# Kernel tuning notes

Measured on AMD Instinct MI355X. Metric: run time of the kernel, lower is better.

## Reference

```python
import jax, jax.numpy as jnp
import numpy as np

DIM = 3072
HEADS = 24
HEAD_DIM = 128
MLP_HIDDEN = 12288
SEQ = 2048
BATCH = 1
EPS = 1e-6


def setup_inputs() -> dict:
    key = jax.random.key(0)
    ks = jax.random.split(key, 12)
    s = 0.02
    return {
        "hidden_states": jax.random.normal(ks[0], (BATCH, SEQ, DIM), jnp.float32),
        "temb": jax.random.normal(ks[1], (BATCH, DIM), jnp.float32),
        "rope_cos": jax.random.uniform(ks[2], (SEQ, HEAD_DIM), jnp.float32),
        "rope_sin": jax.random.uniform(ks[3], (SEQ, HEAD_DIM), jnp.float32),
        # AdaLN-Zero single: Linear(dim -> 3*dim)
        "norm_w": jax.random.normal(ks[4], (3 * DIM, DIM), jnp.float32) * s,
        "norm_b": jnp.zeros((3 * DIM,), jnp.float32),
        # fused QKV + MLP projection: Linear(dim -> 3*dim + mlp_hidden)
        "qkv_mlp_w": jax.random.normal(ks[5], (3 * DIM + MLP_HIDDEN, DIM), jnp.float32) * s,
        "qkv_mlp_b": jnp.zeros((3 * DIM + MLP_HIDDEN,), jnp.float32),
        # proj_out: Linear(dim + mlp_hidden -> dim)
        "proj_w": jax.random.normal(ks[6], (DIM, DIM + MLP_HIDDEN), jnp.float32) * s,
        "proj_b": jnp.zeros((DIM,), jnp.float32),
        # qk RMSNorm weights (per head_dim)
        "rms_q_w": jnp.ones((HEAD_DIM,), jnp.float32),
        "rms_k_w": jnp.ones((HEAD_DIM,), jnp.float32),
    }


def _rms_norm(x, w):
    # x: [B,S,H,D], normalize over D
    var = jnp.mean(jnp.square(x), axis=-1, keepdims=True)
    return x * jax.lax.rsqrt(var + EPS) * w


def _apply_rope(x, cos, sin):
    # x: [B,S,H,D]; cos/sin: [S,D]. diffusers use_real, unbind_dim=-1 convention.
    xr = x.reshape(*x.shape[:-1], HEAD_DIM // 2, 2)
    rot = jnp.stack([-xr[..., 1], xr[..., 0]], axis=-1).reshape(x.shape)
    c = cos[None, :, None, :]
    s = sin[None, :, None, :]
    return x * c + rot * s


def reference(hidden_states, temb, rope_cos, rope_sin, norm_w, norm_b,
              qkv_mlp_w, qkv_mlp_b, proj_w, proj_b, rms_q_w, rms_k_w):
    B, S, _ = hidden_states.shape
    residual = hidden_states

    # --- AdaLayerNormZeroSingle ---
    mod = jax.nn.silu(temb) @ norm_w.T + norm_b          # [B, 3*dim]
    shift, scale, gate = jnp.split(mod, 3, axis=-1)       # each [B, dim]
    mu = jnp.mean(hidden_states, axis=-1, keepdims=True)
    var = jnp.mean(jnp.square(hidden_states - mu), axis=-1, keepdims=True)
    ln = (hidden_states - mu) * jax.lax.rsqrt(var + EPS)
    norm_h = ln * (1.0 + scale[:, None, :]) + shift[:, None, :]

    # --- fused QKV + MLP GEMM ---
    qkv_mlp = norm_h @ qkv_mlp_w.T + qkv_mlp_b             # [B,S,3*dim+mlp]
    qkv, mlp_h = jnp.split(qkv_mlp, [3 * DIM], axis=-1)
    mlp_out = jax.nn.gelu(mlp_h, approximate=True)         # tanh GELU

    q, k, v = jnp.split(qkv, 3, axis=-1)
    q = q.reshape(B, S, HEADS, HEAD_DIM)
    k = k.reshape(B, S, HEADS, HEAD_DIM)
    v = v.reshape(B, S, HEADS, HEAD_DIM)

    # qk RMSNorm + RoPE
    q = _apply_rope(_rms_norm(q, rms_q_w), rope_cos, rope_sin)
    k = _apply_rope(_rms_norm(k, rms_k_w), rope_cos, rope_sin)

    # scaled dot-product attention
    scale_f = 1.0 / np.sqrt(HEAD_DIM)
    scores = jnp.einsum("bqhd,bkhd->bhqk", q, k) * scale_f
    probs = jax.nn.softmax(scores, axis=-1)
    attn = jnp.einsum("bhqk,bkhd->bqhd", probs, v).reshape(B, S, DIM)

    # proj_out on concat(attn, gelu(mlp)) + gated residual
    cat = jnp.concatenate([attn, mlp_out], axis=-1)        # [B,S,dim+mlp]
    proj = cat @ proj_w.T + proj_b                          # [B,S,dim]
    return gate[:, None, :] * proj + residual
```

## Files before the change

### kernel.cpp

```cpp
#include <hip/hip_runtime.h>
#include <stdint.h>

typedef __bf16 bf16;
typedef __bf16 bf16x8 __attribute__((ext_vector_type(8)));
typedef __bf16 bf16x4 __attribute__((ext_vector_type(4)));
typedef float f32x4 __attribute__((ext_vector_type(4)));

#define DIM   3072
#define SEQ   2048
#define QKVW  9216
#define MLPH  12288
#define FUSED 21504
#define CATW  15360
#define HD    128
#define NH    24

__device__ __forceinline__ void gload_lds16(const void* g, void* l) {
  __builtin_amdgcn_global_load_lds((__attribute__((address_space(1))) void*)g,
                                   (__attribute__((address_space(3))) void*)l,
                                   16, 0, 0);
}

__global__ __launch_bounds__(256) void k_mod_gemv(
    const float* __restrict__ temb, const float* __restrict__ nw,
    const float* __restrict__ nb, float* __restrict__ mod)
{
  int j = blockIdx.x * 4 + (threadIdx.x >> 6);
  int lane = threadIdx.x & 63;
  const float* row = nw + (size_t)j * DIM;
  float acc = 0.f;
  #pragma unroll
  for (int k0 = 0; k0 < DIM; k0 += 256) {
    int k = k0 + lane * 4;
    float4 w = *(const float4*)(row + k);
    float4 t = *(const float4*)(temb + k);
    float s0 = t.x / (1.f + __expf(-t.x));
    float s1 = t.y / (1.f + __expf(-t.y));
    float s2 = t.z / (1.f + __expf(-t.z));
    float s3 = t.w / (1.f + __expf(-t.w));
    acc += w.x * s0 + w.y * s1 + w.z * s2 + w.w * s3;
  }
  #pragma unroll
  for (int m = 32; m >= 1; m >>= 1) acc += __shfl_xor(acc, m, 64);
  if (lane == 0) mod[j] = acc + nb[j];
}

__global__ __launch_bounds__(256) void k_ln_mod(
    const float* __restrict__ hs, const float* __restrict__ mod,
    bf16* __restrict__ nh)
{
  int m = blockIdx.x;
  int t = threadIdx.x;
  const float* x = hs + (size_t)m * DIM;
  float4 v[3];
  float s = 0.f, ss = 0.f;
  #pragma unroll
  for (int i = 0; i < 3; i++) {
    v[i] = *(const float4*)(x + i * 1024 + t * 4);
    s  += v[i].x + v[i].y + v[i].z + v[i].w;
    ss += v[i].x * v[i].x + v[i].y * v[i].y + v[i].z * v[i].z + v[i].w * v[i].w;
  }
  #pragma unroll
  for (int msk = 32; msk >= 1; msk >>= 1) {
    s  += __shfl_xor(s, msk, 64);
    ss += __shfl_xor(ss, msk, 64);
  }
  __shared__ float red[8];
  int wave = t >> 6;
  if ((t & 63) == 0) { red[wave] = s; red[4 + wave] = ss; }
  __syncthreads();
  s  = red[0] + red[1] + red[2] + red[3];
  ss = red[4] + red[5] + red[6] + red[7];
  float mu  = s * (1.f / DIM);
  float var = ss * (1.f / DIM) - mu * mu;
  float rstd = rsqrtf(var + 1e-6f);
  #pragma unroll
  for (int i = 0; i < 3; i++) {
    int col = i * 1024 + t * 4;
    const float* sc = mod + DIM + col;
    const float* sh = mod + col;
    float4 vv = v[i];
    bf16x4 o;
    o[0] = (bf16)((vv.x - mu) * rstd * (1.f + sc[0]) + sh[0]);
    o[1] = (bf16)((vv.y - mu) * rstd * (1.f + sc[1]) + sh[1]);
    o[2] = (bf16)((vv.z - mu) * rstd * (1.f + sc[2]) + sh[2]);
    o[3] = (bf16)((vv.w - mu) * rstd * (1.f + sc[3]) + sh[3]);
    *(bf16x4*)(nh + (size_t)m * DIM + col) = o;
  }
}

__global__ __launch_bounds__(256) void k_cvt(
    const float* __restrict__ s, bf16* __restrict__ d, size_t n)
{
  size_t stride = (size_t)gridDim.x * 256 * 8;
  for (size_t i = ((size_t)blockIdx.x * 256 + threadIdx.x) * 8; i < n; i += stride) {
    float4 a = *(const float4*)(s + i);
    float4 b = *(const float4*)(s + i + 4);
    bf16x8 h;
    h[0] = (bf16)a.x; h[1] = (bf16)a.y; h[2] = (bf16)a.z; h[3] = (bf16)a.w;
    h[4] = (bf16)b.x; h[5] = (bf16)b.y; h[6] = (bf16)b.z; h[7] = (bf16)b.w;
    *(bf16x8*)(d + i) = h;
  }
}

template<int MODE>
__global__ __launch_bounds__(512, 2) void k_gemm8(
    const bf16* __restrict__ A, const bf16* __restrict__ B,
    const float* __restrict__ bias, int K, int ntn, int nkp,
    bf16* __restrict__ oq, bf16* __restrict__ ocat, float* __restrict__ pk)
{
  __shared__ bf16 lds[65536];
  int tid = threadIdx.x;
  int wave = tid >> 6, lane = tid & 63;
  int wm = wave >> 2, wn = wave & 3;

  int nwg = gridDim.x;
  int bid = blockIdx.x;
  int swz = (bid & 7) * (nwg >> 3) + (bid >> 3);
  int mt = swz & 7;
  int rest = swz >> 3;
  int nt = rest % ntn;
  int kc = rest / ntn;
  int m0 = mt * 256, n0 = nt * 256;
  int Kp = K / nkp;
  int kbeg = kc * Kp;
  int NT = Kp >> 6;

  int rb0 = (wave >> 1) * 16 + (lane & 15);
  int cb0 = (wave & 1) * 32 + (lane >> 4) * 8;

  const bf16* Ag = A + (size_t)m0 * K + kbeg;
  const bf16* Bg = B + (size_t)n0 * K + kbeg;

  auto stage = [&](const bf16* g0, int kt, int h, int opb) {
    int kw = kt - (kt >= NT ? NT : 0);
    const bf16* g = g0 + (size_t)(h * 128 + rb0) * K + kw * 64 + cb0;
    bf16* l = &lds[((kt & 1) << 15) + opb + ((h << 4) + wave) * 512];
    gload_lds16(g, l);
    gload_lds16(g + (size_t)64 * K, l + 4096);
  };

  f32x4 acc[8][4];
  #pragma unroll
  for (int i = 0; i < 8; i++)
    #pragma unroll
    for (int j = 0; j < 4; j++) acc[i][j] = (f32x4){0.f, 0.f, 0.f, 0.f};

  stage(Ag, 0, 0, 0);     stage(Ag, 0, 1, 0);
  stage(Bg, 0, 0, 16384); stage(Bg, 0, 1, 16384);
  stage(Ag, 1, 0, 0);     stage(Ag, 1, 1, 0);
  asm volatile("s_waitcnt vmcnt(4)" ::: "memory");
  __builtin_amdgcn_s_barrier();

  const int abase = wm * 16 * 512;
  const int bbase = 16384 + wn * 8 * 512;
  const int lo = lane * 8;
  bf16x8 af[8][2], bfr[4][2];

  for (int kt = 0; kt < NT; kt++) {
    int bo = (kt & 1) << 15;
    #pragma unroll
    for (int mi = 0; mi < 4; mi++)
      #pragma unroll
      for (int ks = 0; ks < 2; ks++)
        af[mi][ks] = *(const bf16x8*)&lds[bo + abase + (mi * 2 + ks) * 512 + lo];
    #pragma unroll
    for (int ni = 0; ni < 2; ni++)
      #pragma unroll
      for (int ks = 0; ks < 2; ks++)
        bfr[ni][ks] = *(const bf16x8*)&lds[bo + bbase + (ni * 2 + ks) * 512 + lo];
    stage(Bg, kt + 1, 0, 16384);
    __builtin_amdgcn_s_barrier();
    asm volatile("s_waitcnt lgkmcnt(0)" ::: "memory");
    __builtin_amdgcn_sched_barrier(0);
    __builtin_amdgcn_s_setprio(1);
    #pragma unroll
    for (int mi = 0; mi < 4; mi++)
      #pragma unroll
      for (int ni = 0; ni < 2; ni++)
        #pragma unroll
        for (int ks = 0; ks < 2; ks++)
          acc[mi][ni] = __builtin_amdgcn_mfma_f32_16x16x32_bf16(af[mi][ks], bfr[ni][ks], acc[mi][ni], 0, 0, 0);
    __builtin_amdgcn_s_setprio(0);
    __builtin_amdgcn_s_barrier();
    #pragma unroll
    for (int mi = 4; mi < 8; mi++)
      #pragma unroll
      for (int ks = 0; ks < 2; ks++)
        af[mi][ks] = *(const bf16x8*)&lds[bo + abase + (mi * 2 + ks) * 512 + lo];
    #pragma unroll
    for (int ni = 2; ni < 4; ni++)
      #pragma unroll
      for (int ks = 0; ks < 2; ks++)
        bfr[ni][ks] = *(const bf16x8*)&lds[bo + bbase + (ni * 2 + ks) * 512 + lo];
    stage(Bg, kt + 1, 1, 16384);
    __builtin_amdgcn_s_barrier();
    asm volatile("s_waitcnt lgkmcnt(0)" ::: "memory");
    __builtin_amdgcn_sched_barrier(0);
    __builtin_amdgcn_s_setprio(1);
    #pragma unroll
    for (int mi = 4; mi < 8; mi++)
      #pragma unroll
      for (int ni = 2; ni < 4; ni++)
        #pragma unroll
        for (int ks = 0; ks < 2; ks++)
          acc[mi][ni] = __builtin_amdgcn_mfma_f32_16x16x32_bf16(af[mi][ks], bfr[ni][ks], acc[mi][ni], 0, 0, 0);
    __builtin_amdgcn_s_setprio(0);
    __builtin_amdgcn_s_barrier();
    stage(Ag, kt + 2, 0, 0);
    __builtin_amdgcn_s_barrier();
    __builtin_amdgcn_sched_barrier(0);
    __builtin_amdgcn_s_setprio(1);
    #pragma unroll
    for (int mi = 0; mi < 4; mi++)
      #pragma unroll
      for (int ni = 2; ni < 4; ni++)
        #pragma unroll
        for (int ks = 0; ks < 2; ks++)
          acc[mi][ni] = __builtin_amdgcn_mfma_f32_16x16x32_bf16(af[mi][ks], bfr[ni][ks], acc[mi][ni], 0, 0, 0);
    __builtin_amdgcn_s_setprio(0);
    __builtin_amdgcn_s_barrier();
    stage(Ag, kt + 2, 1, 0);
    asm volatile("s_waitcnt vmcnt(4)" ::: "memory");
    __builtin_amdgcn_s_barrier();
    __builtin_amdgcn_sched_barrier(0);
    __builtin_amdgcn_s_setprio(1);
    #pragma unroll
    for (int mi = 4; mi < 8; mi++)
      #pragma unroll
      for (int ni = 0; ni < 2; ni++)
        #pragma unroll
        for (int ks = 0; ks < 2; ks++)
          acc[mi][ni] = __builtin_amdgcn_mfma_f32_16x16x32_bf16(af[mi][ks], bfr[ni][ks], acc[mi][ni], 0, 0, 0);
    __builtin_amdgcn_s_setprio(0);
    __builtin_amdgcn_s_barrier();
  }

  int rr = (lane >> 4) * 4, cl = lane & 15;
  int mw0 = m0 + wm * 128, nw0 = n0 + wn * 64;
  #pragma unroll
  for (int mi = 0; mi < 8; mi++) {
    #pragma unroll
    for (int ni = 0; ni < 4; ni++) {
      int n = nw0 + ni * 16 + cl;
      #pragma unroll
      for (int r = 0; r < 4; r++) {
        int m = mw0 + mi * 16 + rr + r;
        float v = acc[mi][ni][r];
        if (MODE == 0) {
          v += bias[n];
          if (n < QKVW) {
            oq[(size_t)m * QKVW + n] = (bf16)v;
          } else {
            float g = 0.5f * v * (1.f + tanhf(0.7978845608028654f * (v + 0.044715f * v * v * v)));
            ocat[(size_t)m * CATW + DIM + (n - QKVW)] = (bf16)g;
          }
        } else {
          pk[(size_t)kc * SEQ * DIM + (size_t)m * DIM + n] = v;
        }
      }
    }
  }
}

template<int MODE>
__global__ __launch_bounds__(256) void k_gemm2(
    const bf16* __restrict__ A, const float* __restrict__ Bf,
    const float* __restrict__ bias, int K, int ntn,
    bf16* __restrict__ oq, bf16* __restrict__ ocat,
    const float* __restrict__ gate, const float* __restrict__ resid,
    float* __restrict__ of)
{
  __shared__ bf16 sA[8192];
  __shared__ bf16 sB[8192];
  int nwg = gridDim.x;
  int bid = blockIdx.x;
  int swz = (bid & 7) * (nwg >> 3) + (bid >> 3);
  int mt = swz & 15, nt = swz >> 4;
  int m0 = mt * 128, n0 = nt * 128;
  int tid = threadIdx.x;
  int wave = tid >> 6, lane = tid & 63;
  int wr = wave >> 1, wc = wave & 1;

  size_t aoff[4], boff[4];
  bf16* la[4];
  bf16* lb[4];
  #pragma unroll
  for (int i = 0; i < 4; i++) {
    int c = wave * 4 + i;
    int rt = c >> 1, kt = c & 1;
    int row = rt * 16 + (lane & 15);
    int col = kt * 32 + (lane >> 4) * 8;
    aoff[i] = (size_t)(m0 + row) * K + col;
    boff[i] = (size_t)(n0 + row) * K + col;
    la[i] = sA + c * 512;
    lb[i] = sB + c * 512;
  }
  f32x4 acc[4][4];
  #pragma unroll
  for (int i = 0; i < 4; i++)
    #pragma unroll
    for (int j = 0; j < 4; j++) acc[i][j] = (f32x4){0.f, 0.f, 0.f, 0.f};

  for (int kk = 0; kk < K; kk += 64) {
    #pragma unroll
    for (int i = 0; i < 4; i++)
      gload_lds16(A + aoff[i] + kk, la[i]);
    #pragma unroll
    for (int i = 0; i < 4; i++) {
      const float* g = Bf + boff[i] + kk;
      float4 f0 = *(const float4*)g;
      float4 f1 = *(const float4*)(g + 4);
      bf16x8 h;
      h[0] = (bf16)f0.x; h[1] = (bf16)f0.y; h[2] = (bf16)f0.z; h[3] = (bf16)f0.w;
      h[4] = (bf16)f1.x; h[5] = (bf16)f1.y; h[6] = (bf16)f1.z; h[7] = (bf16)f1.w;
      *(bf16x8*)(lb[i] + lane * 8) = h;
    }
    __syncthreads();
    #pragma unroll
    for (int ks = 0; ks < 2; ks++) {
      bf16x8 af[4], bfr[4];
      #pragma unroll
      for (int mi = 0; mi < 4; mi++)
        af[mi] = *(const bf16x8*)(sA + ((wr * 4 + mi) * 2 + ks) * 512 + lane * 8);
      #pragma unroll
      for (int nj = 0; nj < 4; nj++)
        bfr[nj] = *(const bf16x8*)(sB + ((wc * 4 + nj) * 2 + ks) * 512 + lane * 8);
      #pragma unroll
      for (int mi = 0; mi < 4; mi++)
        #pragma unroll
        for (int nj = 0; nj < 4; nj++)
          acc[mi][nj] = __builtin_amdgcn_mfma_f32_16x16x32_bf16(af[mi], bfr[nj], acc[mi][nj], 0, 0, 0);
    }
    __syncthreads();
  }

  int rr = (lane >> 4) * 4;
  int cl = lane & 15;
  #pragma unroll
  for (int mi = 0; mi < 4; mi++) {
    #pragma unroll
    for (int nj = 0; nj < 4; nj++) {
      int mbase = m0 + wr * 64 + mi * 16 + rr;
      int n = n0 + wc * 64 + nj * 16 + cl;
      #pragma unroll
      for (int r = 0; r < 4; r++) {
        int m = mbase + r;
        float v = acc[mi][nj][r] + bias[n];
        if (MODE == 0) {
          if (n < QKVW) {
            oq[(size_t)m * QKVW + n] = (bf16)v;
          } else {
            float g = 0.5f * v * (1.f + tanhf(0.7978845608028654f * (v + 0.044715f * v * v * v)));
            ocat[(size_t)m * CATW + DIM + (n - QKVW)] = (bf16)g;
          }
        } else {
          of[(size_t)m * DIM + n] = gate[n] * v + resid[(size_t)m * DIM + n];
        }
      }
    }
  }
}

__global__ __launch_bounds__(256) void k_red(
    const float* __restrict__ pk, const float* __restrict__ bias,
    const float* __restrict__ gate, const float* __restrict__ resid,
    float* __restrict__ out)
{
  int m = blockIdx.x / 3;
  int n = (blockIdx.x % 3) * 1024 + threadIdx.x * 4;
  size_t idx = (size_t)m * DIM + n;
  f32x4 p0 = *(const f32x4*)(pk + idx);
  f32x4 p1 = *(const f32x4*)(pk + (size_t)SEQ * DIM + idx);
  f32x4 b  = *(const f32x4*)(bias + n);
  f32x4 g  = *(const f32x4*)(gate + n);
  f32x4 r  = *(const f32x4*)(resid + idx);
  f32x4 o;
  #pragma unroll
  for (int i = 0; i < 4; i++) o[i] = g[i] * (p0[i] + p1[i] + b[i]) + r[i];
  *(f32x4*)(out + idx) = o;
}

__global__ __launch_bounds__(256) void k_rmsrope(
    bf16* __restrict__ qkv, const float* __restrict__ rc, const float* __restrict__ rs,
    const float* __restrict__ qw, const float* __restrict__ kw)
{
  int srow = blockIdx.x >> 1;
  int isk  = blockIdx.x & 1;
  int off  = isk ? DIM : 0;
  const float* w = isk ? kw : qw;
  int g = threadIdx.x >> 5, gl = threadIdx.x & 31;
  int d = gl * 4;
  #pragma unroll
  for (int hh = 0; hh < 3; hh++) {
    int h = g + hh * 8;
    bf16* p = qkv + (size_t)srow * QKVW + off + h * HD + d;
    bf16x4 u = *(const bf16x4*)p;
    float x0 = (float)u[0], x1 = (float)u[1], x2 = (float)u[2], x3 = (float)u[3];
    float ssq = x0 * x0 + x1 * x1 + x2 * x2 + x3 * x3;
    #pragma unroll
    for (int msk = 16; msk >= 1; msk >>= 1) ssq += __shfl_xor(ssq, msk, 32);
    float r = rsqrtf(ssq * (1.f / HD) + 1e-6f);
    float y0 = x0 * r * w[d], y1 = x1 * r * w[d + 1];
    float y2 = x2 * r * w[d + 2], y3 = x3 * r * w[d + 3];
    const float* c = rc + srow * HD + d;
    const float* sn = rs + srow * HD + d;
    bf16x4 o;
    o[0] = (bf16)(y0 * c[0] - y1 * sn[0]);
    o[1] = (bf16)(y1 * c[1] + y0 * sn[1]);
    o[2] = (bf16)(y2 * c[2] - y3 * sn[2]);
    o[3] = (bf16)(y3 * c[3] + y2 * sn[3]);
    *(bf16x4*)p = o;
  }
}

__global__ __launch_bounds__(256) void k_attn(
    const bf16* __restrict__ qkv, bf16* __restrict__ cat)
{
  int h  = blockIdx.y;
  int q0 = blockIdx.x * 64;
  int tid = threadIdx.x, wave = tid >> 6, lane = tid & 63;
  int r16 = lane & 15, g4 = lane >> 4;
  __shared__ bf16 sK[32 * 136];
  __shared__ bf16 sVt[128 * 40];
  __shared__ bf16 sP[4][16 * 40];

  bf16x8 qf[4];
  {
    int qrow = q0 + wave * 16 + r16;
    const bf16* qp = qkv + (size_t)qrow * QKVW + h * HD + g4 * 8;
    #pragma unroll
    for (int kc = 0; kc < 4; kc++) qf[kc] = *(const bf16x8*)(qp + kc * 32);
  }
  f32x4 oacc[8];
  #pragma unroll
  for (int dc = 0; dc < 8; dc++) oacc[dc] = (f32x4){0.f, 0.f, 0.f, 0.f};
  float mrow[4] = {-1e30f, -1e30f, -1e30f, -1e30f};
  float lrow[4] = {0.f, 0.f, 0.f, 0.f};
  const float scale = 0.08838834764831845f;

  for (int kv0 = 0; kv0 < SEQ; kv0 += 32) {
    {
      int row = tid >> 3, c0 = (tid & 7) * 16;
      const bf16* kp = qkv + (size_t)(kv0 + row) * QKVW + DIM + h * HD + c0;
      uint4 a = *(const uint4*)kp;
      uint4 b = *(const uint4*)(kp + 8);
      *(uint4*)&sK[row * 136 + c0]     = a;
      *(uint4*)&sK[row * 136 + c0 + 8] = b;
    }
    {
      int kv = tid >> 3, c0 = (tid & 7) * 16;
      const bf16* vp = qkv + (size_t)(kv0 + kv) * QKVW + 2 * DIM + h * HD + c0;
      #pragma unroll
      for (int i = 0; i < 4; i++) {
        bf16x4 u = *(const bf16x4*)(vp + i * 4);
        sVt[(c0 + i * 4 + 0) * 40 + kv] = u[0];
        sVt[(c0 + i * 4 + 1) * 40 + kv] = u[1];
        sVt[(c0 + i * 4 + 2) * 40 + kv] = u[2];
        sVt[(c0 + i * 4 + 3) * 40 + kv] = u[3];
      }
    }
    __syncthreads();

    f32x4 sv[2];
    sv[0] = (f32x4){0.f, 0.f, 0.f, 0.f};
    sv[1] = (f32x4){0.f, 0.f, 0.f, 0.f};
    #pragma unroll
    for (int ct = 0; ct < 2; ct++)
      #pragma unroll
      for (int kc = 0; kc < 4; kc++) {
        bf16x8 kf = *(const bf16x8*)&sK[(ct * 16 + r16) * 136 + kc * 32 + g4 * 8];
        sv[ct] = __builtin_amdgcn_mfma_f32_16x16x32_bf16(qf[kc], kf, sv[ct], 0, 0, 0);
      }

    bf16* sPw = &sP[wave][0];
    #pragma unroll
    for (int r = 0; r < 4; r++) {
      float a0 = sv[0][r] * scale, a1 = sv[1][r] * scale;
      float mx = fmaxf(a0, a1);
      #pragma unroll
      for (int msk = 8; msk >= 1; msk >>= 1) mx = fmaxf(mx, __shfl_xor(mx, msk, 16));
      float mnew = fmaxf(mrow[r], mx);
      float so = __expf(mrow[r] - mnew);
      float p0 = __expf(a0 - mnew), p1 = __expf(a1 - mnew);
      float rsum = p0 + p1;
      #pragma unroll
      for (int msk = 8; msk >= 1; msk >>= 1) rsum += __shfl_xor(rsum, msk, 16);
      lrow[r] = lrow[r] * so + rsum;
      mrow[r] = mnew;
      #pragma unroll
      for (int dc = 0; dc < 8; dc++) oacc[dc][r] *= so;
      int prow = g4 * 4 + r;
      sPw[prow * 40 + r16]      = (bf16)p0;
      sPw[prow * 40 + 16 + r16] = (bf16)p1;
    }
    asm volatile("s_waitcnt lgkmcnt(0)" ::: "memory");
    __builtin_amdgcn_sched_barrier(0);
    bf16x8 pa = *(const bf16x8*)&sPw[r16 * 40 + g4 * 8];
    #pragma unroll
    for (int dc = 0; dc < 8; dc++) {
      bf16x8 vf = *(const bf16x8*)&sVt[(dc * 16 + r16) * 40 + g4 * 8];
      oacc[dc] = __builtin_amdgcn_mfma_f32_16x16x32_bf16(pa, vf, oacc[dc], 0, 0, 0);
    }
    __syncthreads();
  }

  #pragma unroll
  for (int dc = 0; dc < 8; dc++) {
    #pragma unroll
    for (int r = 0; r < 4; r++) {
      int qrow = q0 + wave * 16 + g4 * 4 + r;
      int col  = h * HD + dc * 16 + r16;
      cat[(size_t)qrow * CATW + col] = (bf16)(oacc[dc][r] / lrow[r]);
    }
  }
}

extern "C" void kernel_launch(void* const* d_in, const int* in_sizes, int n_in,
                              void* d_out, int out_size, void* d_ws, size_t ws_size,
                              hipStream_t stream) {
  const float* hs      = (const float*)d_in[0];
  const float* temb    = (const float*)d_in[1];
  const float* rope_c  = (const float*)d_in[2];
  const float* rope_s  = (const float*)d_in[3];
  const float* norm_w  = (const float*)d_in[4];
  const float* norm_b  = (const float*)d_in[5];
  const float* qkvml_w = (const float*)d_in[6];
  const float* qkvml_b = (const float*)d_in[7];
  const float* proj_w  = (const float*)d_in[8];
  const float* proj_b  = (const float*)d_in[9];
  const float* rms_q_w = (const float*)d_in[10];
  const float* rms_k_w = (const float*)d_in[11];
  float* out = (float*)d_out;

  char* ws = (char*)d_ws;
  size_t off = 0;
  float* mod  = (float*)(ws + off); off += 40960;
  bf16*  nh   = (bf16*)(ws + off); off += (size_t)SEQ * DIM * 2;
  bf16*  qkvb = (bf16*)(ws + off); off += (size_t)SEQ * QKVW * 2;
  bf16*  catb = (bf16*)(ws + off); off += (size_t)SEQ * CATW * 2;
  bf16*  wqb  = (bf16*)(ws + off); off += (size_t)FUSED * DIM * 2;
  bf16*  wpb  = (bf16*)(ws + off); off += (size_t)DIM * CATW * 2;
  float* pkbf = (float*)(ws + off); off += (size_t)2 * SEQ * DIM * 4;
  bool full = (ws_size >= off);

  if (full) {
    k_cvt<<<dim3(2048), dim3(256), 0, stream>>>(qkvml_w, wqb, (size_t)FUSED * DIM);
    k_cvt<<<dim3(2048), dim3(256), 0, stream>>>(proj_w, wpb, (size_t)DIM * CATW);
  }
  k_mod_gemv<<<dim3(QKVW / 4), dim3(256), 0, stream>>>(temb, norm_w, norm_b, mod);
  k_ln_mod<<<dim3(SEQ), dim3(256), 0, stream>>>(hs, mod, nh);

  if (full) {
    k_gemm8<0><<<dim3(8 * (FUSED / 256)), dim3(512), 0, stream>>>(
        nh, wqb, qkvml_b, DIM, FUSED / 256, 1, qkvb, catb, nullptr);
  } else {
    k_gemm2<0><<<dim3(16 * (FUSED / 128)), dim3(256), 0, stream>>>(
        nh, qkvml_w, qkvml_b, DIM, FUSED / 128, qkvb, catb, nullptr, nullptr, nullptr);
  }

  k_rmsrope<<<dim3(SEQ * 2), dim3(256), 0, stream>>>(qkvb, rope_c, rope_s, rms_q_w, rms_k_w);
  k_attn<<<dim3(SEQ / 64, NH), dim3(256), 0, stream>>>(qkvb, catb);

  if (full) {
    k_gemm8<1><<<dim3(8 * (DIM / 256) * 2), dim3(512), 0, stream>>>(
        catb, wpb, nullptr, CATW, DIM / 256, 2, nullptr, nullptr, pkbf);
    k_red<<<dim3(SEQ * 3), dim3(256), 0, stream>>>(pkbf, proj_b, mod + 2 * DIM, hs, out);
  } else {
    k_gemm2<1><<<dim3(16 * (DIM / 128)), dim3(256), 0, stream>>>(
        catb, proj_w, proj_b, CATW, DIM / 128, nullptr, nullptr, mod + 2 * DIM, hs, out);
  }
}
```

Measured before the change: 1.022 ms.

## Restructure GEMM main loop into finer-grained quarter-tile prefetch pipeline unrolled by two

Replaces the half-tile staging lambdas with quarter-granular A/B stagers and unrolls the k-loop by two with explicit buffer offsets. Global-to-LDS loads for the next tiles are interleaved across the four MFMA quadrants, and the wait counts change (vmcnt 6, a partial lgkmcnt 8), so more loads stay in flight while the MFMAs run. The added risk is hazards from the subtler ordering of buffers and barriers, and the loop now assumes NT is even.

```diff
diff --git a/kernel.cpp b/kernel.cpp
--- a/kernel.cpp
+++ b/kernel.cpp
@@ -103,6 +103,8 @@
   }
 }
 
+#define MFMA_B16(a, b, c) __builtin_amdgcn_mfma_f32_16x16x32_bf16(a, b, c, 0, 0, 0)
+
 template<int MODE>
 __global__ __launch_bounds__(512, 2) void k_gemm8(
     const bf16* __restrict__ A, const bf16* __restrict__ B,
@@ -126,19 +128,30 @@
   int kbeg = kc * Kp;
   int NT = Kp >> 6;
 
-  int rb0 = (wave >> 1) * 16 + (lane & 15);
-  int cb0 = (wave & 1) * 32 + (lane >> 4) * 8;
-
   const bf16* Ag = A + (size_t)m0 * K + kbeg;
   const bf16* Bg = B + (size_t)n0 * K + kbeg;
 
-  auto stage = [&](const bf16* g0, int kt, int h, int opb) {
-    int kw = kt - (kt >= NT ? NT : 0);
-    const bf16* g = g0 + (size_t)(h * 128 + rb0) * K + kw * 64 + cb0;
-    bf16* l = &lds[((kt & 1) << 15) + opb + ((h << 4) + wave) * 512];
-    gload_lds16(g, l);
-    gload_lds16(g + (size_t)64 * K, l + 4096);
+  auto stA = [&](int kt, int q) {
+    int kw = kt >= NT ? kt - NT : kt;
+    #pragma unroll
+    for (int j = 0; j < 2; j++) {
+      int c = j * 16 + q * 8 + wave;
+      gload_lds16(Ag + (size_t)((c >> 1) * 16 + (lane & 15)) * K
+                     + ((c & 1) * 32 + (lane >> 4) * 8) + kw * 64,
+                  &lds[((kt & 1) << 15) + c * 512]);
+    }
   };
+  auto stB = [&](int kt, int q) {
+    int kw = kt >= NT ? kt - NT : kt;
+    #pragma unroll
+    for (int j = 0; j < 2; j++) {
+      int v = j * 8 + wave;
+      int c = (v >> 2) * 8 + q * 4 + (v & 3);
+      gload_lds16(Bg + (size_t)((c >> 1) * 16 + (lane & 15)) * K
+                     + ((c & 1) * 32 + (lane >> 4) * 8) + kw * 64,
+                  &lds[((kt & 1) << 15) + 16384 + c * 512]);
+    }
+  };
 
   f32x4 acc[8][4];
   #pragma unroll
@@ -146,94 +159,81 @@
     #pragma unroll
     for (int j = 0; j < 4; j++) acc[i][j] = (f32x4){0.f, 0.f, 0.f, 0.f};
 
-  stage(Ag, 0, 0, 0);     stage(Ag, 0, 1, 0);
-  stage(Bg, 0, 0, 16384); stage(Bg, 0, 1, 16384);
-  stage(Ag, 1, 0, 0);     stage(Ag, 1, 1, 0);
-  asm volatile("s_waitcnt vmcnt(4)" ::: "memory");
-  __builtin_amdgcn_s_barrier();
-
-  const int abase = wm * 16 * 512;
-  const int bbase = 16384 + wn * 8 * 512;
+  const int abase = wm * 8192;
+  const int bbase = 16384 + wn * 4096;
   const int lo = lane * 8;
   bf16x8 af[8][2], bfr[4][2];
 
-  for (int kt = 0; kt < NT; kt++) {
-    int bo = (kt & 1) << 15;
-    #pragma unroll
-    for (int mi = 0; mi < 4; mi++)
-      #pragma unroll
-      for (int ks = 0; ks < 2; ks++)
-        af[mi][ks] = *(const bf16x8*)&lds[bo + abase + (mi * 2 + ks) * 512 + lo];
-    #pragma unroll
-    for (int ni = 0; ni < 2; ni++)
-      #pragma unroll
-      for (int ks = 0; ks < 2; ks++)
-        bfr[ni][ks] = *(const bf16x8*)&lds[bo + bbase + (ni * 2 + ks) * 512 + lo];
-    stage(Bg, kt + 1, 0, 16384);
-    __builtin_amdgcn_s_barrier();
-    asm volatile("s_waitcnt lgkmcnt(0)" ::: "memory");
-    __builtin_amdgcn_sched_barrier(0);
-    __builtin_amdgcn_s_setprio(1);
-    #pragma unroll
-    for (int mi = 0; mi < 4; mi++)
-      #pragma unroll
-      for (int ni = 0; ni < 2; ni++)
-        #pragma unroll
-        for (int ks = 0; ks < 2; ks++)
-          acc[mi][ni] = __builtin_amdgcn_mfma_f32_16x16x32_bf16(af[mi][ks], bfr[ni][ks], acc[mi][ni], 0, 0, 0);
+  #define RD_A(MI0, BO) \
+    _Pragma("unroll") for (int mi = 0; mi < 4; mi++) \
+    _Pragma("unroll") for (int ks = 0; ks < 2; ks++) \
+      af[MI0 + mi][ks] = *(const bf16x8*)&lds[(BO) + abase + ((MI0 + mi) * 2 + ks) * 512 + lo];
+  #define RD_B(NI0, BO) \
+    _Pragma("unroll") for (int ni = 0; ni < 2; ni++) \
+    _Pragma("unroll") for (int ks = 0; ks < 2; ks++) \
+      bfr[NI0 + ni][ks] = *(const bf16x8*)&lds[(BO) + bbase + ((NI0 + ni) * 2 + ks) * 512 + lo];
+  #define QUAD(MI0, NI0) \
+    __builtin_amdgcn_s_setprio(1); \
+    _Pragma("unroll") for (int mi = 0; mi < 4; mi++) \
+    _Pragma("unroll") for (int ni = 0; ni < 2; ni++) \
+    _Pragma("unroll") for (int ks = 0; ks < 2; ks++) \
+      acc[MI0 + mi][NI0 + ni] = MFMA_B16(af[MI0 + mi][ks], bfr[NI0 + ni][ks], acc[MI0 + mi][NI0 + ni]); \
     __builtin_amdgcn_s_setprio(0);
-    __builtin_amdgcn_s_barrier();
-    #pragma unroll
-    for (int mi = 4; mi < 8; mi++)
-      #pragma unroll
-      for (int ks = 0; ks < 2; ks++)
-        af[mi][ks] = *(const bf16x8*)&lds[bo + abase + (mi * 2 + ks) * 512 + lo];
-    #pragma unroll
-    for (int ni = 2; ni < 4; ni++)
-      #pragma unroll
-      for (int ks = 0; ks < 2; ks++)
-        bfr[ni][ks] = *(const bf16x8*)&lds[bo + bbase + (ni * 2 + ks) * 512 + lo];
-    stage(Bg, kt + 1, 1, 16384);
-    __builtin_amdgcn_s_barrier();
-    asm volatile("s_waitcnt lgkmcnt(0)" ::: "memory");
-    __builtin_amdgcn_sched_barrier(0);
-    __builtin_amdgcn_s_setprio(1);
-    #pragma unroll
-    for (int mi = 4; mi < 8; mi++)
-      #pragma unroll
-      for (int ni = 2; ni < 4; ni++)
-        #pragma unroll
-        for (int ks = 0; ks < 2; ks++)
-          acc[mi][ni] = __builtin_amdgcn_mfma_f32_16x16x32_bf16(af[mi][ks], bfr[ni][ks], acc[mi][ni], 0, 0, 0);
-    __builtin_amdgcn_s_setprio(0);
-    __builtin_amdgcn_s_barrier();
-    stage(Ag, kt + 2, 0, 0);
-    __builtin_amdgcn_s_barrier();
-    __builtin_amdgcn_sched_barrier(0);
-    __builtin_amdgcn_s_setprio(1);
-    #pragma unroll
-    for (int mi = 0; mi < 4; mi++)
-      #pragma unroll
-      for (int ni = 2; ni < 4; ni++)
-        #pragma unroll
-        for (int ks = 0; ks < 2; ks++)
-          acc[mi][ni] = __builtin_amdgcn_mfma_f32_16x16x32_bf16(af[mi][ks], bfr[ni][ks], acc[mi][ni], 0, 0, 0);
-    __builtin_amdgcn_s_setprio(0);
-    __builtin_amdgcn_s_barrier();
-    stage(Ag, kt + 2, 1, 0);
-    asm volatile("s_waitcnt vmcnt(4)" ::: "memory");
-    __builtin_amdgcn_s_barrier();
-    __builtin_amdgcn_sched_barrier(0);
-    __builtin_amdgcn_s_setprio(1);
-    #pragma unroll
-    for (int mi = 4; mi < 8; mi++)
-      #pragma unroll
-      for (int ni = 0; ni < 2; ni++)
-        #pragma unroll
-        for (int ks = 0; ks < 2; ks++)
-          acc[mi][ni] = __builtin_amdgcn_mfma_f32_16x16x32_bf16(af[mi][ks], bfr[ni][ks], acc[mi][ni], 0, 0, 0);
-    __builtin_amdgcn_s_setprio(0);
-    __builtin_amdgcn_s_barrier();
+  #define BAR()   __builtin_amdgcn_s_barrier()
+  #define LGKM0() asm volatile("s_waitcnt lgkmcnt(0)" ::: "memory")
+  #define LGKM8() asm volatile("s_waitcnt lgkmcnt(8)" ::: "memory")
+  #define VM6()   asm volatile("s_waitcnt vmcnt(6)" ::: "memory")
+  #define SB0()   __builtin_amdgcn_sched_barrier(0)
+
+  stA(0, 0); stB(0, 0); stA(0, 1); stB(0, 1);
+  stA(1, 0); stB(1, 0); stA(1, 1);
+  VM6();
+  BAR();
+
+  for (int it = 0; it < NT; it += 2) {
+    int ta = it, tb = it + 1;
+    RD_A(0, 0) RD_B(0, 0)
+    stB(tb, 1);
+    LGKM8();
+    BAR(); LGKM0(); SB0();
+    QUAD(0, 0)
+    BAR();
+    RD_A(4, 0)
+    stA(ta + 2, 0);
+    BAR(); LGKM0(); SB0();
+    QUAD(4, 0)
+    BAR();
+    RD_B(2, 0)
+    stB(ta + 2, 0);
+    BAR(); LGKM0(); SB0();
+    QUAD(0, 2)
+    BAR();
+    stA(ta + 2, 1);
+    VM6();
+    BAR(); SB0();
+    QUAD(4, 2)
+    BAR();
+    RD_A(0, 32768) RD_B(0, 32768)
+    stB(ta + 2, 1);
+    LGKM8();
+    BAR(); LGKM0(); SB0();
+    QUAD(0, 0)
+    BAR();
+    RD_A(4, 32768)
+    stA(tb + 2, 0);
+    BAR(); LGKM0(); SB0();
+    QUAD(4, 0)
+    BAR();
+    RD_B(2, 32768)
+    stB(tb + 2, 0);
+    BAR(); LGKM0(); SB0();
+    QUAD(0, 2)
+    BAR();
+    stA(tb + 2, 1);
+    VM6();
+    BAR(); SB0();
+    QUAD(4, 2)
+    BAR();
   }
 
   int rr = (lane >> 4) * 4, cl = lane & 15;
```

Result: no change. 1.019 ms (-0.3%).
